# Kernel tuning notes

Measured on AMD Instinct MI355X. Metric: run time of the kernel, lower is better.

The kernel has to match this reference:

```python
import jax, jax.numpy as jnp
import numpy as np

B, L, H, G, NH, DH, FF = 16, 512, 1024, 2, 16, 64, 4096
DM = H // G          # per-group d_model = 512
LG = L // G          # inner attention seq len = 256
EPS = 1e-6


def _ln(x, g, b):
    m = x.mean(-1, keepdims=True)
    v = ((x - m) ** 2).mean(-1, keepdims=True)
    return (x - m) * jax.lax.rsqrt(v + EPS) * g + b


def setup_inputs() -> dict:
    key = jax.random.key(0)
    ks = jax.random.split(key, 12)
    sd = 0.02
    n = lambda k, sh: jax.random.normal(k, sh, jnp.float32) * sd
    return {
        "y": jax.random.normal(ks[0], (B, L, H), jnp.float32),
        "y_mask": jax.random.randint(ks[1], (B, 1, 1, LG), 0, 2).astype(bool),
        # MHAtt projections (operate on per-group d_model = DM)
        "Wv": n(ks[2], (DM, DM)), "bv": jnp.zeros((DM,), jnp.float32),
        "Wk": n(ks[3], (DM, DM)), "bk": jnp.zeros((DM,), jnp.float32),
        "Wq": n(ks[4], (DM, DM)), "bq": jnp.zeros((DM,), jnp.float32),
        # merge projection (full hidden)
        "Wm": n(ks[5], (H, H)), "bm": jnp.zeros((H,), jnp.float32),
        # GFFN: linear1 H->FF, linear2 grouped FF/G -> H/G
        "W1": n(ks[6], (H, FF)), "b1": jnp.zeros((FF,), jnp.float32),
        "W2": n(ks[7], (FF // G, H // G)), "b2": jnp.zeros((H // G,), jnp.float32),
        # LayerNorms
        "g1": jnp.ones((H,), jnp.float32), "beta1": jnp.zeros((H,), jnp.float32),
        "g2": jnp.ones((H,), jnp.float32), "beta2": jnp.zeros((H,), jnp.float32),
    }


def reference(y, y_mask, Wv, bv, Wk, bk, Wq, bq, Wm, bm, W1, b1, W2, b2,
              g1, beta1, g2, beta2):
    b, l, d = y.shape
    # group reshuffle: split channels into G groups, stack along batch
    yg = jnp.concatenate(jnp.split(y, G, axis=-1), axis=0)        # (b*G, l, DM)
    mask = jnp.tile(y_mask, (G, 1, 1, 1))                          # (b*G, 1, 1, l/G)

    # projections; view uses h*dh = H so inner seq becomes l/G
    q = (yg @ Wq + bq).reshape(b * G, -1, NH, DH).transpose(0, 2, 1, 3)  # (bG, NH, l/G, DH)
    k = (yg @ Wk + bk).reshape(b * G, -1, NH, DH).transpose(0, 2, 1, 3)
    v = (yg @ Wv + bv).reshape(b * G, -1, NH, DH).transpose(0, 2, 1, 3)

    scores = jnp.einsum('bhqd,bhkd->bhqk', q, k) / np.sqrt(DH)
    scores = jnp.where(mask, jnp.float32(-1e9), scores)
    att = jax.nn.softmax(scores, axis=-1)                          # dropout = identity (eval)
    ctx = jnp.einsum('bhqk,bhkd->bhqd', att, v)                    # (bG, NH, l/G, DH)
    ctx = ctx.transpose(0, 2, 1, 3).reshape(b * G, -1, DM)         # (bG, l, DM)

    atted = jnp.concatenate(jnp.split(ctx, G, axis=0), axis=-1)    # (b, l, H)
    atted = atted @ Wm + bm
    y1 = _ln(y + atted, g1, beta1)

    # GFFN
    h1 = jax.nn.relu(y1 @ W1 + b1)                                  # (b, l, FF)
    h2 = jnp.einsum('blgf,fo->blgo', h1.reshape(b, l, G, FF // G), W2) + b2
    ff = h2.reshape(b, l, H)
    return _ln(y1 + ff, g2, beta2)
```

## Files before the change

kernel.cpp:

```cpp
#include <hip/hip_runtime.h>
#include <stdint.h>

typedef unsigned short u16;
using us8   = __attribute__((ext_vector_type(8))) unsigned short;
using us4   = __attribute__((ext_vector_type(4))) unsigned short;
using bf16x8 = __attribute__((ext_vector_type(8))) __bf16;
using f32x4 = __attribute__((ext_vector_type(4))) float;

#define DEV static __device__ __forceinline__

DEV float bf2f(u16 u) { union { uint32_t i; float f; } v; v.i = (uint32_t)u << 16; return v.f; }
DEV u16 f2bf(float f) {
    union { float f; uint32_t i; } v; v.f = f;
    uint32_t u = v.i;
    return (u16)((u + 0x7FFFu + ((u >> 16) & 1u)) >> 16);
}

DEV void async16(const u16* g, u16* ldsbase)
{
    __builtin_amdgcn_global_load_lds((const __attribute__((address_space(1))) void*)g,
                                     (__attribute__((address_space(3))) void*)ldsbase, 16, 0, 0);
}

struct DetectArgs { const void* p[18]; int nw[18]; };

__global__ __launch_bounds__(256) void k_detect_all(DetectArgs a, int* flags)
{
    const int b = blockIdx.x;
    const int t = threadIdx.x;
    __shared__ int cnt[4];
    if (t < 4) cnt[t] = 0;
    __syncthreads();
    if (b == 1) {
        const uint8_t* m = (const uint8_t*)a.p[1];
        int c0 = 0, c1 = 0, c2 = 0, c3 = 0;
        for (int i = t; i < 4096; i += 256) {
            uint8_t v = m[i];
            int mod = i & 3;
            if (v == 0x3F && mod == 1) c0++;
            if (v == 0x3F && mod == 3) c1++;
            if (v == 1 && mod != 0) c2++;
            if (v == 1 && mod == 0) c3++;
        }
        atomicAdd(&cnt[0], c0); atomicAdd(&cnt[1], c1); atomicAdd(&cnt[2], c2); atomicAdd(&cnt[3], c3);
        __syncthreads();
        if (t == 0) {
            int mf;
            if (cnt[0] > 0) mf = 2;
            else if (cnt[1] > 0) mf = 3;
            else if (cnt[2] > 0) mf = 0;
            else if (cnt[3] > 0) mf = 1;
            else mf = 0;
            flags[1] = mf;
        }
    } else {
        const u16* p = (const u16*)a.p[b];
        int nw = a.nw[b];
        int nze = 0, pe = 0, nzo = 0;
        for (int i = t; i < nw; i += 256) {
            u16 w = p[i];
            if (w == 0) continue;
            int e = (w >> 7) & 0xFF;
            bool pl = (e >= 90 && e <= 140);
            if ((i & 1) == 0) { nze++; if (pl) pe++; }
            else nzo++;
        }
        atomicAdd(&cnt[0], nze); atomicAdd(&cnt[1], pe); atomicAdd(&cnt[2], nzo);
        __syncthreads();
        if (t == 0) {
            int f;
            if (cnt[0] > 0)      f = (cnt[1] * 10 >= cnt[0] * 6) ? 2 : 3;
            else if (cnt[2] > 0) f = 3;
            else                 f = 2;
            flags[b] = f;
        }
    }
}

__global__ __launch_bounds__(256) void k_expand_mask(const void* mask, const int* flag, float* mb)
{
    int i = blockIdx.x * 256 + threadIdx.x;
    if (i >= 4096) return;
    int f = *flag;
    bool on;
    if (f == 0)      on = ((const uint8_t*)mask)[i]  != 0;
    else if (f == 1) on = ((const int*)mask)[i]      != 0;
    else if (f == 2) on = ((const u16*)mask)[i]      != 0;
    else             on = ((const uint32_t*)mask)[i] != 0;
    mb[i] = on ? -1e9f : 0.0f;
}

__global__ __launch_bounds__(256) void k_convert_bf(const void* src, u16* dst, int n, const int* flag)
{
    int i = blockIdx.x * 256 + threadIdx.x;
    if (i >= n) return;
    if (*flag == 2) dst[i] = ((const u16*)src)[i];
    else            dst[i] = f2bf(((const float*)src)[i]);
}

struct TransArgs { const void* src[6]; u16* dst[6]; int R[6]; int C[6]; int flagidx[6]; int tstart[7]; };

__global__ __launch_bounds__(256) void k_transpose_all(TransArgs a, const int* flags)
{
    const int tb = blockIdx.x;
    int s = 0;
    while (tb >= a.tstart[s + 1]) s++;
    const int lt = tb - a.tstart[s];
    const int R = a.R[s], C = a.C[s];
    const int tilesX = C >> 5;
    const int ti = lt / tilesX, tj = lt - ti * tilesX;
    const int r0 = ti * 32, c0 = tj * 32;
    const bool isbf = (flags[a.flagidx[s]] == 2);
    const int t = threadIdx.x;
    const int j = t & 31, i0 = t >> 5;
    __shared__ u16 tile[32][33];
#pragma unroll
    for (int p = 0; p < 4; p++) {
        int r = r0 + i0 + p * 8;
        size_t idx = (size_t)r * C + c0 + j;
        u16 v = isbf ? ((const u16*)a.src[s])[idx] : f2bf(((const float*)a.src[s])[idx]);
        tile[i0 + p * 8][j] = v;
    }
    __syncthreads();
    u16* dst = a.dst[s];
#pragma unroll
    for (int p = 0; p < 4; p++) {
        int c = i0 + p * 8;
        dst[(size_t)(c0 + c) * R + r0 + j] = tile[j][c];
    }
}

struct ConvArgs { const void* src[10]; int flagidx[10]; int off[10]; int n[10]; };

__global__ __launch_bounds__(256) void k_convert_params(ConvArgs a, const int* flags, float* par)
{
    int i = blockIdx.x * 256 + threadIdx.x;
    if (i >= 11264) return;
    int s = 0;
    while (s < 9 && i >= a.off[s] + a.n[s]) s++;
    int j = i - a.off[s];
    float v;
    if (flags[a.flagidx[s]] == 2) v = bf2f(((const u16*)a.src[s])[j]);
    else                          v = ((const float*)a.src[s])[j];
    par[i] = v;
}

template<int BM, int BN, int WR, int WC, int TM, int TN>
DEV void gemm_tile(const u16* __restrict__ A, int lda,
                   const u16* __restrict__ Bt, int ldb, int K,
                   u16* As, u16* Bs, f32x4 (&acc)[TM][TN])
{
    const int t = threadIdx.x;
    const int lane = t & 63;
    const int wave = t >> 6;
    const int wr = wave / WC;
    const int wc = wave % WC;
    const int m16 = lane & 15;
    const int quad = lane >> 4;
    const int lr8 = lane >> 3;
    const int lsw = (((lane & 7) ^ lr8) << 3);

#pragma unroll
    for (int i = 0; i < TM; i++)
#pragma unroll
        for (int j = 0; j < TN; j++) {
            acc[i][j][0] = 0.f; acc[i][j][1] = 0.f; acc[i][j][2] = 0.f; acc[i][j][3] = 0.f;
        }

    for (int kb = 0; kb < K; kb += 64) {
#pragma unroll
        for (int i = 0; i < BM / 32; i++) {
            int chunk = wave * (BM / 32) + i;
            int r = chunk * 8 + lr8;
            async16(A + (size_t)r * lda + kb + lsw, As + chunk * 512);
        }
#pragma unroll
        for (int i = 0; i < BN / 32; i++) {
            int chunk = wave * (BN / 32) + i;
            int r = chunk * 8 + lr8;
            async16(Bt + (size_t)r * ldb + kb + lsw, Bs + chunk * 512);
        }
        __syncthreads();
#pragma unroll
        for (int ks = 0; ks < 2; ks++) {
            bf16x8 af[TM], bfr[TN];
#pragma unroll
            for (int i = 0; i < TM; i++) {
                int row = wr * TM * 16 + i * 16 + m16;
                int jq = ks * 4 + quad;
                af[i] = *(const bf16x8*)(As + row * 64 + ((jq ^ (row & 7)) << 3));
            }
#pragma unroll
            for (int j = 0; j < TN; j++) {
                int row = wc * TN * 16 + j * 16 + m16;
                int jq = ks * 4 + quad;
                bfr[j] = *(const bf16x8*)(Bs + row * 64 + ((jq ^ (row & 7)) << 3));
            }
#pragma unroll
            for (int i = 0; i < TM; i++)
#pragma unroll
                for (int j = 0; j < TN; j++)
                    acc[i][j] = __builtin_amdgcn_mfma_f32_16x16x32_bf16(af[i], bfr[j], acc[i][j], 0, 0, 0);
        }
        __syncthreads();
    }
}

template<bool RELU>
__global__ __launch_bounds__(256) void k_gemm_std(const u16* __restrict__ A, int lda,
                                                  const u16* __restrict__ Bt, int ldb,
                                                  const float* __restrict__ bias,
                                                  u16* __restrict__ C, int ldc, int K)
{
    __shared__ __align__(16) u16 As[128 * 64];
    __shared__ __align__(16) u16 Bs[128 * 64];
    const u16* Ab = A + (size_t)blockIdx.y * 128 * lda;
    const u16* Bb = Bt + (size_t)blockIdx.x * 128 * ldb;
    f32x4 acc[4][4];
    gemm_tile<128, 128, 2, 2, 4, 4>(Ab, lda, Bb, ldb, K, As, Bs, acc);

    const int t = threadIdx.x, lane = t & 63, wave = t >> 6;
    const int wr = wave >> 1, wc = wave & 1, m16 = lane & 15, quad = lane >> 4;
    const size_t rowBase = (size_t)blockIdx.y * 128 + wr * 64;
    const int colBase = blockIdx.x * 128 + wc * 64;
#pragma unroll
    for (int tm = 0; tm < 4; tm++)
#pragma unroll
        for (int tn = 0; tn < 4; tn++) {
            int col = colBase + tn * 16 + m16;
            float bv = bias ? bias[col] : 0.f;
#pragma unroll
            for (int r = 0; r < 4; r++) {
                size_t row = rowBase + tm * 16 + quad * 4 + r;
                float v = acc[tm][tn][r] + bv;
                if (RELU) v = fmaxf(v, 0.f);
                C[row * (size_t)ldc + col] = f2bf(v);
            }
        }
}

__global__ __launch_bounds__(512, 2) void k_qkv_attn(const u16* __restrict__ y_c,
                                                     const u16* __restrict__ WqT,
                                                     const u16* __restrict__ WkT,
                                                     const u16* __restrict__ WvT,
                                                     const float* __restrict__ par,
                                                     const float* __restrict__ maskb,
                                                     u16* __restrict__ attedpre)
{
    __shared__ __align__(16) u16 smem[49152];
    u16* As  = smem;
    u16* Wqs = smem + 16384;
    u16* Wks = smem + 20480;
    u16* Wvs = smem + 24576;
    u16* Ks  = smem;
    u16* Vs  = smem + 16384;
    u16* Pw8 = smem + 32768;

    const int z = blockIdx.x;
    const int bg = z >> 4, h = z & 15, hbit = h >> 3, hlow = h & 7;
    const int b = bg & 15, g = bg >> 4;
    const int t = threadIdx.x, lane = t & 63, wave = t >> 6;
    const int m16 = lane & 15, quad = lane >> 4;
    const int lr8 = lane >> 3;
    const int lsw = (((lane & 7) ^ lr8) << 3);

    const u16* Yb = y_c + (size_t)(b * 512 + hbit) * 1024 + g * 512;

    f32x4 aq[2][4], ak[2][4], av[2][4];
#pragma unroll
    for (int i = 0; i < 2; i++)
#pragma unroll
        for (int j = 0; j < 4; j++) {
            aq[i][j][0]=0.f; aq[i][j][1]=0.f; aq[i][j][2]=0.f; aq[i][j][3]=0.f;
            ak[i][j][0]=0.f; ak[i][j][1]=0.f; ak[i][j][2]=0.f; ak[i][j][3]=0.f;
            av[i][j][0]=0.f; av[i][j][1]=0.f; av[i][j][2]=0.f; av[i][j][3]=0.f;
        }

    for (int c = 0; c < 8; ++c) {
        const int kb = c * 64;
#pragma unroll
        for (int i = 0; i < 4; i++) {
            int chunk = wave * 4 + i;
            int srow = chunk * 8 + lr8;
            async16(Yb + (size_t)srow * 2048 + kb + lsw, As + chunk * 512);
        }
        {
            int row = wave * 8 + lr8;
            const size_t woff = (size_t)(hlow * 64 + row) * 512 + kb + lsw;
            async16(WqT + woff, Wqs + wave * 512);
            async16(WkT + woff, Wks + wave * 512);
            async16(WvT + woff, Wvs + wave * 512);
        }
        __syncthreads();
#pragma unroll
        for (int ks = 0; ks < 2; ks++) {
            const int jq = ks * 4 + quad;
            bf16x8 af[2];
#pragma unroll
            for (int mt = 0; mt < 2; mt++) {
                int row = wave * 32 + mt * 16 + m16;
                af[mt] = *(const bf16x8*)(As + row * 64 + ((jq ^ (row & 7)) << 3));
            }
#pragma unroll
            for (int tn = 0; tn < 4; tn++) {
                int rowb = tn * 16 + m16;
                int offb = rowb * 64 + ((jq ^ (rowb & 7)) << 3);
                bf16x8 wq = *(const bf16x8*)(Wqs + offb);
                bf16x8 wk = *(const bf16x8*)(Wks + offb);
                bf16x8 wv = *(const bf16x8*)(Wvs + offb);
#pragma unroll
                for (int mt = 0; mt < 2; mt++) {
                    aq[mt][tn] = __builtin_amdgcn_mfma_f32_16x16x32_bf16(af[mt], wq, aq[mt][tn], 0, 0, 0);
                    ak[mt][tn] = __builtin_amdgcn_mfma_f32_16x16x32_bf16(af[mt], wk, ak[mt][tn], 0, 0, 0);
                    av[mt][tn] = __builtin_amdgcn_mfma_f32_16x16x32_bf16(af[mt], wv, av[mt][tn], 0, 0, 0);
                }
            }
        }
        __syncthreads();
    }

    float bQ[4], bK[4], bV[4];
#pragma unroll
    for (int tn = 0; tn < 4; tn++) {
        int c0 = hlow * 64 + tn * 16 + m16;
        bQ[tn] = par[c0]; bK[tn] = par[512 + c0]; bV[tn] = par[1024 + c0];
    }
    u16* Qw = Pw8 + wave * 2048;
#pragma unroll
    for (int tm = 0; tm < 2; tm++)
#pragma unroll
        for (int tn = 0; tn < 4; tn++) {
            int dh = tn * 16 + m16;
#pragma unroll
            for (int r = 0; r < 4; r++) {
                int sl = tm * 16 + quad * 4 + r;
                int s_ = wave * 32 + sl;
                Ks[s_ * 64 + ((((dh >> 3) ^ (s_ & 7)) << 3) | (dh & 7))] = f2bf(ak[tm][tn][r] + bK[tn]);
                {
                    int j = s_ >> 3;
                    int slot = (j & 24) | ((j & 7) ^ (dh & 7));
                    Vs[dh * 256 + slot * 8 + (s_ & 7)] = f2bf(av[tm][tn][r] + bV[tn]);
                }
                Qw[sl * 64 + ((((dh >> 3) ^ (sl & 7)) << 3) | (dh & 7))] = f2bf(aq[tm][tn][r] + bQ[tn]);
            }
        }
    bf16x8 qf[2][2];
#pragma unroll
    for (int mt = 0; mt < 2; mt++)
#pragma unroll
        for (int ks = 0; ks < 2; ks++) {
            int row = mt * 16 + m16;
            int jq = ks * 4 + quad;
            qf[mt][ks] = *(const bf16x8*)(Qw + row * 64 + ((jq ^ (row & 7)) << 3));
        }
    float mb[16];
#pragma unroll
    for (int nt = 0; nt < 16; nt++) mb[nt] = maskb[b * 256 + nt * 16 + m16];

    __syncthreads();

    f32x4 s[2][16];
#pragma unroll
    for (int mt = 0; mt < 2; mt++)
#pragma unroll
        for (int nt = 0; nt < 16; nt++) { s[mt][nt][0]=0.f; s[mt][nt][1]=0.f; s[mt][nt][2]=0.f; s[mt][nt][3]=0.f; }
#pragma unroll
    for (int ks = 0; ks < 2; ks++) {
        int jq = ks * 4 + quad;
#pragma unroll
        for (int nt = 0; nt < 16; nt++) {
            int row = nt * 16 + m16;
            bf16x8 kf = *(const bf16x8*)(Ks + row * 64 + ((jq ^ (row & 7)) << 3));
#pragma unroll
            for (int mt = 0; mt < 2; mt++)
                s[mt][nt] = __builtin_amdgcn_mfma_f32_16x16x32_bf16(qf[mt][ks], kf, s[mt][nt], 0, 0, 0);
        }
    }

    float rinv[2][4];
#pragma unroll
    for (int mt = 0; mt < 2; mt++)
#pragma unroll
        for (int r = 0; r < 4; r++) {
            float mm = -3.0e38f;
#pragma unroll
            for (int nt = 0; nt < 16; nt++) {
                float v = s[mt][nt][r] * 0.125f + mb[nt];
                s[mt][nt][r] = v;
                mm = fmaxf(mm, v);
            }
            mm = fmaxf(mm, __shfl_xor(mm, 1));
            mm = fmaxf(mm, __shfl_xor(mm, 2));
            mm = fmaxf(mm, __shfl_xor(mm, 4));
            mm = fmaxf(mm, __shfl_xor(mm, 8));
            float ss = 0.f;
#pragma unroll
            for (int nt = 0; nt < 16; nt++) {
                float e = __expf(s[mt][nt][r] - mm);
                s[mt][nt][r] = e;
                ss += e;
            }
            ss += __shfl_xor(ss, 1);
            ss += __shfl_xor(ss, 2);
            ss += __shfl_xor(ss, 4);
            ss += __shfl_xor(ss, 8);
            rinv[mt][r] = 1.0f / ss;
        }

    f32x4 ctx[2][4];
#pragma unroll
    for (int mt = 0; mt < 2; mt++)
#pragma unroll
        for (int dt = 0; dt < 4; dt++) { ctx[mt][dt][0]=0.f; ctx[mt][dt][1]=0.f; ctx[mt][dt][2]=0.f; ctx[mt][dt][3]=0.f; }

#pragma unroll
    for (int kc = 0; kc < 4; kc++) {
#pragma unroll
        for (int mt = 0; mt < 2; mt++)
#pragma unroll
            for (int nl = 0; nl < 4; nl++) {
                int nt = kc * 4 + nl;
#pragma unroll
                for (int r = 0; r < 4; r++) {
                    int row = mt * 16 + quad * 4 + r;
                    int col = nl * 16 + m16;
                    int j = col >> 3, e = col & 7;
                    Qw[row * 64 + (((j ^ (row & 7)) << 3) | e)] = f2bf(s[mt][nt][r] * rinv[mt][r]);
                }
            }
#pragma unroll
        for (int ks = 0; ks < 2; ks++) {
            int jq = ks * 4 + quad;
            bf16x8 pf[2];
#pragma unroll
            for (int mt = 0; mt < 2; mt++) {
                int row = mt * 16 + m16;
                pf[mt] = *(const bf16x8*)(Qw + row * 64 + ((jq ^ (row & 7)) << 3));
            }
#pragma unroll
            for (int dt = 0; dt < 4; dt++) {
                int d = dt * 16 + m16;
                int j = kc * 8 + ks * 4 + quad;
                int slot = (j & 24) | ((j & 7) ^ (d & 7));
                bf16x8 vf = *(const bf16x8*)(Vs + d * 256 + slot * 8);
#pragma unroll
                for (int mt = 0; mt < 2; mt++)
                    ctx[mt][dt] = __builtin_amdgcn_mfma_f32_16x16x32_bf16(pf[mt], vf, ctx[mt][dt], 0, 0, 0);
            }
        }
    }

    const int cBase = g * 512 + hlow * 64;
#pragma unroll
    for (int mt = 0; mt < 2; mt++)
#pragma unroll
        for (int dt = 0; dt < 4; dt++) {
            int dh = dt * 16 + m16;
#pragma unroll
            for (int r = 0; r < 4; r++) {
                int sI = wave * 32 + mt * 16 + quad * 4 + r;
                int l = 2 * sI + hbit;
                attedpre[((size_t)b * 512 + l) * 1024 + cBase + dh] = f2bf(ctx[mt][dt][r]);
            }
        }
}

__global__ __launch_bounds__(256) void k_gemm_ffn2(const u16* __restrict__ h1,
                                                   const u16* __restrict__ W2T,
                                                   const float* __restrict__ b2,
                                                   u16* __restrict__ out)
{
    __shared__ __align__(16) u16 As[128 * 64];
    __shared__ __align__(16) u16 Bs[128 * 64];
    const int xi = blockIdx.x;
    const int g = xi >> 2, xn = xi & 3;
    const u16* Ab = h1 + (size_t)blockIdx.y * 128 * 4096 + g * 2048;
    const u16* Bb = W2T + (size_t)xn * 128 * 2048;
    f32x4 acc[4][4];
    gemm_tile<128, 128, 2, 2, 4, 4>(Ab, 4096, Bb, 2048, 2048, As, Bs, acc);

    const int t = threadIdx.x, lane = t & 63, wave = t >> 6;
    const int wr = wave >> 1, wc = wave & 1, m16 = lane & 15, quad = lane >> 4;
    const size_t rowBase = (size_t)blockIdx.y * 128 + wr * 64;
    const int colg = xn * 128 + wc * 64;
#pragma unroll
    for (int tm = 0; tm < 4; tm++)
#pragma unroll
        for (int tn = 0; tn < 4; tn++) {
            int cg = colg + tn * 16 + m16;
            float bv = b2[cg];
#pragma unroll
            for (int r = 0; r < 4; r++) {
                size_t row = rowBase + tm * 16 + quad * 4 + r;
                out[row * 1024 + g * 512 + cg] = f2bf(acc[tm][tn][r] + bv);
            }
        }
}

template<int FINAL>
__global__ __launch_bounds__(256) void k_ln(const u16* __restrict__ x1, const u16* __restrict__ x2,
                                            const float* __restrict__ gamma, const float* __restrict__ beta,
                                            void* __restrict__ outv, const int* __restrict__ yflag)
{
    const size_t row = blockIdx.x;
    const int t = threadIdx.x;
    us4 a = *(const us4*)(x1 + row * 1024 + t * 4);
    us4 b = *(const us4*)(x2 + row * 1024 + t * 4);
    float v[4]; float s = 0.f, s2 = 0.f;
#pragma unroll
    for (int i = 0; i < 4; i++) { v[i] = bf2f(a[i]) + bf2f(b[i]); s += v[i]; s2 += v[i] * v[i]; }
#pragma unroll
    for (int off = 32; off > 0; off >>= 1) { s += __shfl_xor(s, off); s2 += __shfl_xor(s2, off); }
    __shared__ float red[8];
    const int lane = t & 63, wave = t >> 6;
    if (lane == 0) { red[wave] = s; red[wave + 4] = s2; }
    __syncthreads();
    s = red[0] + red[1] + red[2] + red[3];
    s2 = red[4] + red[5] + red[6] + red[7];
    float mean = s * (1.0f / 1024.0f);
    float var = fmaxf(s2 * (1.0f / 1024.0f) - mean * mean, 0.0f);
    float rs = rsqrtf(var + 1e-6f);
    float o[4];
#pragma unroll
    for (int i = 0; i < 4; i++) {
        int c = t * 4 + i;
        o[i] = (v[i] - mean) * rs * gamma[c] + beta[c];
    }
    bool f32out = FINAL && yflag && (*yflag == 3);
    if (f32out) {
        float* out = (float*)outv;
#pragma unroll
        for (int i = 0; i < 4; i++) out[row * 1024 + t * 4 + i] = o[i];
    } else {
        u16* out = (u16*)outv;
        us4 ov;
#pragma unroll
        for (int i = 0; i < 4; i++) ov[i] = f2bf(o[i]);
        *(us4*)(out + row * 1024 + t * 4) = ov;
    }
}

extern "C" void kernel_launch(void* const* d_in, const int* in_sizes, int n_in,
                              void* d_out, int out_size, void* d_ws, size_t ws_size,
                              hipStream_t stream)
{
    (void)in_sizes; (void)n_in; (void)out_size; (void)ws_size;
    const void* y    = d_in[0];
    const void* mask = d_in[1];
    const void* Wv = d_in[2];  const void* bv = d_in[3];
    const void* Wk = d_in[4];  const void* bk = d_in[5];
    const void* Wq = d_in[6];  const void* bq = d_in[7];
    const void* Wm = d_in[8];  const void* bm = d_in[9];
    const void* W1 = d_in[10]; const void* b1 = d_in[11];
    const void* W2 = d_in[12]; const void* b2 = d_in[13];
    const void* g1 = d_in[14]; const void* be1 = d_in[15];
    const void* g2 = d_in[16]; const void* be2 = d_in[17];

    char* ws = (char*)d_ws;
    size_t off = 0;
    auto alloc = [&](size_t bytes) { void* p = ws + off; off = (off + bytes + 255) & ~(size_t)255; return p; };

    int*   flags = (int*)alloc(32 * 4);
    float* maskb = (float*)alloc(16 * 256 * 4);
    float* par   = (float*)alloc(11264 * 4);
    u16* WqT  = (u16*)alloc((size_t)262144 * 2);
    u16* WkT  = (u16*)alloc((size_t)262144 * 2);
    u16* WvT  = (u16*)alloc((size_t)262144 * 2);
    u16* WmT  = (u16*)alloc((size_t)1048576 * 2);
    u16* W1T  = (u16*)alloc((size_t)4194304 * 2);
    u16* W2T  = (u16*)alloc((size_t)1048576 * 2);
    u16* y_c  = (u16*)alloc((size_t)8388608 * 2);
    u16* slotA = (u16*)alloc((size_t)8388608 * 2);
    u16* slotB = (u16*)alloc((size_t)8388608 * 2);
    u16* slotC = (u16*)alloc((size_t)8388608 * 2);
    u16* slotD = (u16*)alloc((size_t)8388608 * 2);
    u16* Pbig  = (u16*)alloc((size_t)33554432 * 2);

    float* p_bm  = par + 1536;
    float* p_b1  = par + 2560;
    float* p_b2  = par + 6656;
    float* p_g1  = par + 7168;
    float* p_be1 = par + 8192;
    float* p_g2  = par + 9216;
    float* p_be2 = par + 10240;

    DetectArgs da;
    {
        const void* srcs[18] = {y, mask, Wv, bv, Wk, bk, Wq, bq, Wm, bm, W1, b1, W2, b2, g1, be1, g2, be2};
        const int   nele[18] = {8388608, 4096, 262144, 512, 262144, 512, 262144, 512, 1048576, 1024,
                                4194304, 4096, 1048576, 512, 1024, 1024, 1024, 1024};
        for (int i = 0; i < 18; i++) { da.p[i] = srcs[i]; da.nw[i] = nele[i] < 4096 ? nele[i] : 4096; }
    }
    k_detect_all<<<18, 256, 0, stream>>>(da, flags);

    k_expand_mask<<<16, 256, 0, stream>>>(mask, flags + 1, maskb);
    k_convert_bf<<<32768, 256, 0, stream>>>(y, y_c, 8388608, flags + 0);

    TransArgs ta;
    {
        const void* s6[6] = {Wq, Wk, Wv, Wm, W1, W2};
        u16* d6[6] = {WqT, WkT, WvT, WmT, W1T, W2T};
        int R6[6] = {512, 512, 512, 1024, 1024, 2048};
        int C6[6] = {512, 512, 512, 1024, 4096, 512};
        int f6[6] = {6, 4, 2, 8, 10, 12};
        int ts[7] = {0, 256, 512, 768, 1792, 5888, 6912};
        for (int i = 0; i < 6; i++) { ta.src[i] = s6[i]; ta.dst[i] = d6[i]; ta.R[i] = R6[i]; ta.C[i] = C6[i]; ta.flagidx[i] = f6[i]; }
        for (int i = 0; i < 7; i++) ta.tstart[i] = ts[i];
    }
    k_transpose_all<<<6912, 256, 0, stream>>>(ta, flags);

    ConvArgs ca;
    {
        const void* s10[10] = {bq, bk, bv, bm, b1, b2, g1, be1, g2, be2};
        int f10[10] = {7, 5, 3, 9, 11, 13, 14, 15, 16, 17};
        int o10[10] = {0, 512, 1024, 1536, 2560, 6656, 7168, 8192, 9216, 10240};
        int n10[10] = {512, 512, 512, 1024, 4096, 512, 1024, 1024, 1024, 1024};
        for (int i = 0; i < 10; i++) { ca.src[i] = s10[i]; ca.flagidx[i] = f10[i]; ca.off[i] = o10[i]; ca.n[i] = n10[i]; }
    }
    k_convert_params<<<44, 256, 0, stream>>>(ca, flags, par);

    u16* attedpre = slotD;
    k_qkv_attn<<<512, 512, 0, stream>>>(y_c, WqT, WkT, WvT, par, maskb, attedpre);

    u16* mergeout = slotA;
    k_gemm_std<false><<<dim3(8, 64), 256, 0, stream>>>(attedpre, 1024, WmT, 1024, p_bm, mergeout, 1024, 1024);

    u16* y1 = slotB;
    k_ln<0><<<8192, 256, 0, stream>>>(y_c, mergeout, p_g1, p_be1, y1, nullptr);

    u16* h1 = Pbig;
    k_gemm_std<true><<<dim3(32, 64), 256, 0, stream>>>(y1, 1024, W1T, 1024, p_b1, h1, 4096, 1024);

    u16* ffout = slotC;
    k_gemm_ffn2<<<dim3(8, 64), 256, 0, stream>>>(h1, W2T, p_b2, ffout);

    k_ln<1><<<8192, 256, 0, stream>>>(y1, ffout, p_g2, p_be2, d_out, flags + 0);
}
```

Before: 415.4 us.

## Add 256x256 ping-pong MFMA GEMM for first half of FFN1 rows

Adds a new 512-thread GEMM kernel with 256x256 output tiles, a double-buffered global-to-LDS async load pipeline, XOR-swizzled LDS, and interleaved staging between MFMA quarters under setprio. The FFN linear1 GEMM is split: the first 4096 rows use the new large-tile kernel (256 blocks, one per CU), and the remaining rows use the existing 128x128 kernel. The goal is more operand reuse per LDS load and better overlap of loads with MFMA work. In exchange it adds a second launch and a higher register and LDS footprint, which lowers occupancy.

```diff
diff --git a/kernel.cpp b/kernel.cpp
--- a/kernel.cpp
+++ b/kernel.cpp
@@ -239,6 +239,174 @@
         }
 }
 
+template<bool RELU>
+__global__ __launch_bounds__(512, 2) void k_gemm256p(const u16* __restrict__ A, int lda,
+                                                     const u16* __restrict__ Bt, int ldb,
+                                                     const float* __restrict__ bias,
+                                                     u16* __restrict__ C, int ldc, int K)
+{
+    __shared__ __align__(16) u16 As[2][256 * 64];
+    __shared__ __align__(16) u16 Bs[2][256 * 64];
+    const int t = threadIdx.x;
+    const int lane = t & 63, wave = t >> 6;
+    const int wr = wave >> 2, wc = wave & 3;
+    const int m16 = lane & 15, quad = lane >> 4;
+    const int lr8 = lane >> 3;
+    const int lsw = (((lane & 7) ^ lr8) << 3);
+
+    const u16* __restrict__ Ab = A + (size_t)blockIdx.y * 256 * lda;
+    const u16* __restrict__ Bb = Bt + (size_t)blockIdx.x * 256 * ldb;
+
+    f32x4 acc[8][4];
+#pragma unroll
+    for (int i = 0; i < 8; i++)
+#pragma unroll
+        for (int j = 0; j < 4; j++) {
+            acc[i][j][0] = 0.f; acc[i][j][1] = 0.f; acc[i][j][2] = 0.f; acc[i][j][3] = 0.f;
+        }
+
+    const int NT = K >> 6;
+
+    auto stage_region = [&](int kb, int c, int h) {
+        const bool isA = (h < 2);
+        const u16* src = isA ? Ab : Bb;
+        const int ld   = isA ? lda : ldb;
+        u16* dst = isA ? &As[c][0] : &Bs[c][0];
+#pragma unroll
+        for (int r = 0; r < 2; r++) {
+            int sub = wave * 2 + r;
+            int chunk = isA ? ((sub & 7) + ((sub >> 3) << 4) + ((h & 1) << 3))
+                            : ((sub & 3) + ((sub >> 2) << 3) + ((h & 1) << 2));
+            int row = chunk * 8 + lr8;
+            async16(src + (size_t)row * ld + kb + lsw, dst + chunk * 512);
+        }
+    };
+
+#pragma unroll
+    for (int h = 0; h < 4; h++) stage_region(0, 0, h);
+    if (NT > 1) {
+#pragma unroll
+        for (int h = 0; h < 4; h++) stage_region(64, 1, h);
+        asm volatile("s_waitcnt vmcnt(8)" ::: "memory");
+    } else {
+        asm volatile("s_waitcnt vmcnt(0)" ::: "memory");
+    }
+    asm volatile("s_barrier" ::: "memory");
+
+    bf16x8 af[2][4], bf0[2][2], bf1[2][2];
+    for (int kt = 0; kt < NT; ++kt) {
+        const int c = kt & 1;
+        const bool pf = (kt + 2 < NT);
+        const int kb2 = (kt + 2) << 6;
+
+#pragma unroll
+        for (int ks = 0; ks < 2; ks++) {
+            int jq = ks * 4 + quad;
+#pragma unroll
+            for (int i = 0; i < 4; i++) {
+                int row = wr * 128 + 64 + i * 16 + m16;
+                af[ks][i] = *(const bf16x8*)(&As[c][row * 64 + ((jq ^ (row & 7)) << 3)]);
+            }
+#pragma unroll
+            for (int j = 0; j < 2; j++) {
+                int row = wc * 64 + j * 16 + m16;
+                bf0[ks][j] = *(const bf16x8*)(&Bs[c][row * 64 + ((jq ^ (row & 7)) << 3)]);
+            }
+        }
+        asm volatile("s_barrier" ::: "memory");
+        __builtin_amdgcn_s_setprio(1);
+#pragma unroll
+        for (int ks = 0; ks < 2; ks++)
+#pragma unroll
+            for (int i = 0; i < 4; i++)
+#pragma unroll
+                for (int j = 0; j < 2; j++)
+                    acc[4 + i][j] = __builtin_amdgcn_mfma_f32_16x16x32_bf16(af[ks][i], bf0[ks][j],
+                                                                            acc[4 + i][j], 0, 0, 0);
+        __builtin_amdgcn_s_setprio(0);
+        asm volatile("s_barrier" ::: "memory");
+
+        if (pf) { stage_region(kb2, c, 1); stage_region(kb2, c, 2); }
+#pragma unroll
+        for (int ks = 0; ks < 2; ks++) {
+            int jq = ks * 4 + quad;
+#pragma unroll
+            for (int j = 0; j < 2; j++) {
+                int row = wc * 64 + 32 + j * 16 + m16;
+                bf1[ks][j] = *(const bf16x8*)(&Bs[c][row * 64 + ((jq ^ (row & 7)) << 3)]);
+            }
+        }
+        asm volatile("s_barrier" ::: "memory");
+        __builtin_amdgcn_s_setprio(1);
+#pragma unroll
+        for (int ks = 0; ks < 2; ks++)
+#pragma unroll
+            for (int i = 0; i < 4; i++)
+#pragma unroll
+                for (int j = 0; j < 2; j++)
+                    acc[4 + i][2 + j] = __builtin_amdgcn_mfma_f32_16x16x32_bf16(af[ks][i], bf1[ks][j],
+                                                                                acc[4 + i][2 + j], 0, 0, 0);
+        __builtin_amdgcn_s_setprio(0);
+        asm volatile("s_barrier" ::: "memory");
+
+        if (pf) stage_region(kb2, c, 3);
+#pragma unroll
+        for (int ks = 0; ks < 2; ks++) {
+            int jq = ks * 4 + quad;
+#pragma unroll
+            for (int i = 0; i < 4; i++) {
+                int row = wr * 128 + i * 16 + m16;
+                af[ks][i] = *(const bf16x8*)(&As[c][row * 64 + ((jq ^ (row & 7)) << 3)]);
+            }
+        }
+        asm volatile("s_barrier" ::: "memory");
+        __builtin_amdgcn_s_setprio(1);
+#pragma unroll
+        for (int ks = 0; ks < 2; ks++)
+#pragma unroll
+            for (int i = 0; i < 4; i++)
+#pragma unroll
+                for (int j = 0; j < 2; j++)
+                    acc[i][2 + j] = __builtin_amdgcn_mfma_f32_16x16x32_bf16(af[ks][i], bf1[ks][j],
+                                                                            acc[i][2 + j], 0, 0, 0);
+        __builtin_amdgcn_s_setprio(0);
+        asm volatile("s_barrier" ::: "memory");
+
+        if (pf) stage_region(kb2, c, 0);
+        asm volatile("s_barrier" ::: "memory");
+        __builtin_amdgcn_s_setprio(1);
+#pragma unroll
+        for (int ks = 0; ks < 2; ks++)
+#pragma unroll
+            for (int i = 0; i < 4; i++)
+#pragma unroll
+                for (int j = 0; j < 2; j++)
+                    acc[i][j] = __builtin_amdgcn_mfma_f32_16x16x32_bf16(af[ks][i], bf0[ks][j],
+                                                                        acc[i][j], 0, 0, 0);
+        __builtin_amdgcn_s_setprio(0);
+        if (pf) asm volatile("s_waitcnt vmcnt(8)" ::: "memory");
+        else    asm volatile("s_waitcnt vmcnt(0)" ::: "memory");
+        asm volatile("s_barrier" ::: "memory");
+    }
+
+    const size_t rowBase = (size_t)blockIdx.y * 256 + wr * 128;
+    const int colBase = blockIdx.x * 256 + wc * 64;
+#pragma unroll
+    for (int f = 0; f < 8; f++)
+#pragma unroll
+        for (int tn = 0; tn < 4; tn++) {
+            int col = colBase + tn * 16 + m16;
+            float bv = bias ? bias[col] : 0.f;
+#pragma unroll
+            for (int r = 0; r < 4; r++) {
+                size_t row = rowBase + f * 16 + quad * 4 + r;
+                float v = acc[f][tn][r] + bv;
+                if (RELU) v = fmaxf(v, 0.f);
+                C[row * (size_t)ldc + col] = f2bf(v);
+            }
+        }
+}
+
 __global__ __launch_bounds__(512, 2) void k_qkv_attn(const u16* __restrict__ y_c,
                                                      const u16* __restrict__ WqT,
                                                      const u16* __restrict__ WkT,
@@ -629,7 +797,9 @@
     k_ln<0><<<8192, 256, 0, stream>>>(y_c, mergeout, p_g1, p_be1, y1, nullptr);
 
     u16* h1 = Pbig;
-    k_gemm_std<true><<<dim3(32, 64), 256, 0, stream>>>(y1, 1024, W1T, 1024, p_b1, h1, 4096, 1024);
+    k_gemm256p<true><<<dim3(16, 16), 512, 0, stream>>>(y1, 1024, W1T, 1024, p_b1, h1, 4096, 1024);
+    k_gemm_std<true><<<dim3(32, 32), 256, 0, stream>>>(y1 + (size_t)4096 * 1024, 1024, W1T, 1024, p_b1,
+                                                       h1 + (size_t)4096 * 4096, 4096, 1024);
 
     u16* ffout = slotC;
     k_gemm_ffn2<<<dim3(8, 64), 256, 0, stream>>>(h1, W2T, p_b2, ffout);
```

New measurement: 422.2 us. No clear change (+1.6%).

## Double-buffer QKV projection loads and remap block index for weight locality

Applied to the files above, without the earlier changes.

Adds a double-buffered LDS pipeline to the QKV projection loop of the fused attention kernel, issuing the next chunk's async global-to-LDS loads before computing on the current one, with explicit vmcnt waits and raw barriers. It also remaps blockIdx so groups of 8 consecutive blocks share the same head slice of the weights, which may improve L2 reuse. LDS grows from 96KB to 112KB per block, which could limit occupancy under launch_bounds(512,2). The hand-written waitcnt values depend on the exact number of outstanding loads per thread.

```diff
diff --git a/kernel.cpp b/kernel.cpp
--- a/kernel.cpp
+++ b/kernel.cpp
@@ -247,17 +247,19 @@
                                                      const float* __restrict__ maskb,
                                                      u16* __restrict__ attedpre)
 {
-    __shared__ __align__(16) u16 smem[49152];
-    u16* As  = smem;
-    u16* Wqs = smem + 16384;
-    u16* Wks = smem + 20480;
-    u16* Wvs = smem + 24576;
-    u16* Ks  = smem;
-    u16* Vs  = smem + 16384;
-    u16* Pw8 = smem + 32768;
-
-    const int z = blockIdx.x;
-    const int bg = z >> 4, h = z & 15, hbit = h >> 3, hlow = h & 7;
+    __shared__ __align__(16) u16 smem[57344];
+    u16* Asb0 = smem;
+    u16* Asb1 = smem + 16384;
+    u16* Wsb0 = smem + 32768;
+    u16* Wsb1 = smem + 45056;
+    u16* Ks   = smem;
+    u16* Vs   = smem + 16384;
+    u16* Pw8  = smem + 32768;
+
+    const int wg = blockIdx.x;
+    const int grp = (wg >> 6) * 8 + (wg & 7);
+    const int hlow = (wg >> 3) & 7;
+    const int bg = grp >> 1, hbit = grp & 1;
     const int b = bg & 15, g = bg >> 4;
     const int t = threadIdx.x, lane = t & 63, wave = t >> 6;
     const int m16 = lane & 15, quad = lane >> 4;
@@ -276,22 +278,34 @@
             av[i][j][0]=0.f; av[i][j][1]=0.f; av[i][j][2]=0.f; av[i][j][3]=0.f;
         }
 
-    for (int c = 0; c < 8; ++c) {
+    auto stage = [&](int c) {
         const int kb = c * 64;
+        u16* As_ = (c & 1) ? Asb1 : Asb0;
+        u16* Ws_ = (c & 1) ? Wsb1 : Wsb0;
 #pragma unroll
         for (int i = 0; i < 4; i++) {
             int chunk = wave * 4 + i;
             int srow = chunk * 8 + lr8;
-            async16(Yb + (size_t)srow * 2048 + kb + lsw, As + chunk * 512);
-        }
-        {
-            int row = wave * 8 + lr8;
-            const size_t woff = (size_t)(hlow * 64 + row) * 512 + kb + lsw;
-            async16(WqT + woff, Wqs + wave * 512);
-            async16(WkT + woff, Wks + wave * 512);
-            async16(WvT + woff, Wvs + wave * 512);
-        }
-        __syncthreads();
+            async16(Yb + (size_t)srow * 2048 + kb + lsw, As_ + chunk * 512);
+        }
+        int row = wave * 8 + lr8;
+        const size_t woff = (size_t)(hlow * 64 + row) * 512 + kb + lsw;
+        async16(WqT + woff, Ws_ + wave * 512);
+        async16(WkT + woff, Ws_ + 4096 + wave * 512);
+        async16(WvT + woff, Ws_ + 8192 + wave * 512);
+    };
+
+    stage(0);
+    for (int c = 0; c < 8; ++c) {
+        if (c + 1 < 8) {
+            stage(c + 1);
+            asm volatile("s_waitcnt vmcnt(7)" ::: "memory");
+        } else {
+            asm volatile("s_waitcnt vmcnt(0)" ::: "memory");
+        }
+        asm volatile("s_barrier" ::: "memory");
+        const u16* As_ = (c & 1) ? Asb1 : Asb0;
+        const u16* Ws_ = (c & 1) ? Wsb1 : Wsb0;
 #pragma unroll
         for (int ks = 0; ks < 2; ks++) {
             const int jq = ks * 4 + quad;
@@ -299,15 +313,15 @@
 #pragma unroll
             for (int mt = 0; mt < 2; mt++) {
                 int row = wave * 32 + mt * 16 + m16;
-                af[mt] = *(const bf16x8*)(As + row * 64 + ((jq ^ (row & 7)) << 3));
+                af[mt] = *(const bf16x8*)(As_ + row * 64 + ((jq ^ (row & 7)) << 3));
             }
 #pragma unroll
             for (int tn = 0; tn < 4; tn++) {
                 int rowb = tn * 16 + m16;
                 int offb = rowb * 64 + ((jq ^ (rowb & 7)) << 3);
-                bf16x8 wq = *(const bf16x8*)(Wqs + offb);
-                bf16x8 wk = *(const bf16x8*)(Wks + offb);
-                bf16x8 wv = *(const bf16x8*)(Wvs + offb);
+                bf16x8 wq = *(const bf16x8*)(Ws_ + offb);
+                bf16x8 wk = *(const bf16x8*)(Ws_ + 4096 + offb);
+                bf16x8 wv = *(const bf16x8*)(Ws_ + 8192 + offb);
 #pragma unroll
                 for (int mt = 0; mt < 2; mt++) {
                     aq[mt][tn] = __builtin_amdgcn_mfma_f32_16x16x32_bf16(af[mt], wq, aq[mt][tn], 0, 0, 0);
@@ -316,7 +330,7 @@
                 }
             }
         }
-        __syncthreads();
+        asm volatile("s_barrier" ::: "memory");
     }
 
     float bQ[4], bK[4], bV[4];
```

Measured after the change: 396.5 us. 1.05x faster.
